# Kernel tuning notes

Measured on AMD Instinct MI355X. Metric: run time of the kernel, lower is better.

The kernel has to match this reference:

```python
import jax, jax.numpy as jnp
import numpy as np
import math

B, S, D = 2, 2048, 1024
H, KV, HD = 16, 4, 64
N_REP = H // KV
ROPE_THETA = 1.0e6


def _rope_tables(seq_len, head_dim, theta):
    inv_freq = 1.0 / (theta ** (np.arange(0, head_dim, 2, dtype=np.float32) / head_dim))
    t = np.arange(seq_len, dtype=np.float32)
    freqs = np.outer(t, inv_freq)                      # [S, HD/2]
    emb = np.concatenate([freqs, freqs], axis=-1)      # [S, HD]
    return jnp.asarray(np.cos(emb)), jnp.asarray(np.sin(emb))


def setup_inputs() -> dict:
    key = jax.random.key(0)
    ks = jax.random.split(key, 6)
    cos, sin = _rope_tables(S, HD, ROPE_THETA)
    scale = 0.02
    return {
        "x": jax.random.normal(ks[0], (B, S, D), dtype=jnp.float32),
        "cos": cos,
        "sin": sin,
        "Wq": jax.random.normal(ks[1], (D, H * HD), dtype=jnp.float32) * scale,
        "Wk": jax.random.normal(ks[2], (D, KV * HD), dtype=jnp.float32) * scale,
        "Wv": jax.random.normal(ks[3], (D, KV * HD), dtype=jnp.float32) * scale,
        "Wo": jax.random.normal(ks[4], (H * HD, D), dtype=jnp.float32) * scale,
    }


def _rotate_half(u):
    u1, u2 = u[..., : HD // 2], u[..., HD // 2 :]
    return jnp.concatenate([-u2, u1], axis=-1)


def reference(x, cos, sin, Wq, Wk, Wv, Wo):
    bsz, seq_len, _ = x.shape
    q = (x @ Wq).reshape(bsz, seq_len, H, HD)   # [B,S,H,HD]
    k = (x @ Wk).reshape(bsz, seq_len, KV, HD)  # [B,S,KV,HD]
    v = (x @ Wv).reshape(bsz, seq_len, KV, HD)

    # RoPE: cos/sin [S,HD] broadcast over batch and heads (unsqueeze_dim=1)
    c = cos[:seq_len][None, :, None, :]
    s = sin[:seq_len][None, :, None, :]
    q = q * c + _rotate_half(q) * s
    k = k * c + _rotate_half(k) * s

    # repeat_kv: expand KV heads groupwise to H heads
    k = jnp.repeat(k, N_REP, axis=2)  # [B,S,H,HD]
    v = jnp.repeat(v, N_REP, axis=2)

    q = q.transpose(0, 2, 1, 3)  # [B,H,S,HD]
    k = k.transpose(0, 2, 1, 3)
    v = v.transpose(0, 2, 1, 3)

    scores = jnp.einsum("bhqd,bhkd->bhqk", q, k) / math.sqrt(HD)
    causal = jnp.tril(jnp.ones((seq_len, seq_len), dtype=bool))
    scores = jnp.where(causal[None, None], scores, jnp.finfo(jnp.float32).min)
    probs = jax.nn.softmax(scores.astype(jnp.float32), axis=-1).astype(x.dtype)

    out = jnp.einsum("bhqk,bhkd->bhqd", probs, v)        # [B,H,S,HD]
    out = out.transpose(0, 2, 1, 3).reshape(bsz, seq_len, H * HD)
    return out @ Wo
```

## Files before the change

### kernel.cpp

```cpp
#include <hip/hip_runtime.h>

#define SS 2048
#define NH 16
#define NKV 4
#define HD 64

typedef __bf16 bf16;
typedef __bf16 bf16x8 __attribute__((ext_vector_type(8)));
typedef float f32x4 __attribute__((ext_vector_type(4)));

#define SM_SCALE 0.18033688011f

__device__ __forceinline__ void gl_lds16(const bf16* g, bf16* l) {
    __builtin_amdgcn_global_load_lds((const __attribute__((address_space(1))) void*)g,
                                     (__attribute__((address_space(3))) void*)l, 16, 0, 0);
}

__global__ __launch_bounds__(256) void prep_kernel(
    const float* __restrict__ x, const float* __restrict__ Wq, const float* __restrict__ Wk,
    const float* __restrict__ Wv, const float* __restrict__ Wo,
    bf16* __restrict__ xb, bf16* __restrict__ wqkv_t, bf16* __restrict__ wo_t)
{
    const int blk = blockIdx.x;
    const int tid = threadIdx.x;
    if (blk >= 640) {
        const float4* xv = (const float4*)x;
        const size_t base = (size_t)(blk - 640) * 2048 + tid;
        #pragma unroll
        for (int j = 0; j < 8; ++j) {
            const float4 v = xv[base + j * 256];
            bf16* o = xb + (base + j * 256) * 4;
            o[0] = (bf16)v.x; o[1] = (bf16)v.y; o[2] = (bf16)v.z; o[3] = (bf16)v.w;
        }
        return;
    }
    const float* W; bf16* Wt; int N, n0, k0;
    if (blk < 256)      { W = Wq; Wt = wqkv_t;                       N = 1024; n0 = (blk & 15) * 64;         k0 = (blk >> 4) * 64; }
    else if (blk < 320) { W = Wk; Wt = wqkv_t + (size_t)1024 * 1024; N = 256;  n0 = ((blk - 256) & 3) * 64;  k0 = ((blk - 256) >> 2) * 64; }
    else if (blk < 384) { W = Wv; Wt = wqkv_t + (size_t)1280 * 1024; N = 256;  n0 = ((blk - 320) & 3) * 64;  k0 = ((blk - 320) >> 2) * 64; }
    else                { W = Wo; Wt = wo_t;                         N = 1024; n0 = ((blk - 384) & 15) * 64; k0 = ((blk - 384) >> 4) * 64; }

    __shared__ float Ts[64][65];
    const int c = tid & 63, rr = tid >> 6;
    #pragma unroll
    for (int i = 0; i < 16; ++i) {
        const int kk = i * 4 + rr;
        Ts[kk][c] = W[(size_t)(k0 + kk) * N + n0 + c];
    }
    __syncthreads();
    #pragma unroll
    for (int i = 0; i < 16; ++i) {
        const int nn = i * 4 + rr;
        Wt[(size_t)(n0 + nn) * 1024 + k0 + c] = (bf16)Ts[c][nn];
    }
}

template<int EPI>
__global__ __launch_bounds__(512) void gemm_bt_kernel(
    const bf16* __restrict__ A, const bf16* __restrict__ Bt, float* __restrict__ C,
    const float* __restrict__ cosp, const float* __restrict__ sinp,
    bf16* __restrict__ qo, bf16* __restrict__ ko, bf16* __restrict__ vto,
    int M, int N, int K)
{
    __shared__ bf16 As[128 * 32];
    __shared__ bf16 Bs[128 * 32];
    const int m0 = blockIdx.x * 128, n0 = blockIdx.y * 128;
    const int tid = threadIdx.x;
    const int w = tid >> 6, lane = tid & 63, g = lane >> 4, li = lane & 15;
    const int wm = w >> 1, wn = w & 1;

    f32x4 acc[2][4];
    const f32x4 z = {0.f, 0.f, 0.f, 0.f};
    #pragma unroll
    for (int i = 0; i < 2; ++i)
        #pragma unroll
        for (int j = 0; j < 4; ++j) acc[i][j] = z;

    const int srow = tid >> 2, schunk = (tid & 3) * 8;
    const bf16* pA = A + (size_t)(m0 + srow) * K + schunk;
    const bf16* pB = Bt + (size_t)(n0 + srow) * K + schunk;
    bf16* lA = As + (size_t)w * 512;
    bf16* lB = Bs + (size_t)w * 512;

    for (int kk = 0; kk < K; kk += 32) {
        __syncthreads();
        gl_lds16(pA + kk, lA);
        gl_lds16(pB + kk, lB);
        __syncthreads();
        bf16x8 af[2], bfr[4];
        #pragma unroll
        for (int mi = 0; mi < 2; ++mi) af[mi] = *(const bf16x8*)&As[(wm * 32 + mi * 16 + li) * 32 + g * 8];
        #pragma unroll
        for (int ni = 0; ni < 4; ++ni) bfr[ni] = *(const bf16x8*)&Bs[(wn * 64 + ni * 16 + li) * 32 + g * 8];
        #pragma unroll
        for (int mi = 0; mi < 2; ++mi)
            #pragma unroll
            for (int ni = 0; ni < 4; ++ni)
                acc[mi][ni] = __builtin_amdgcn_mfma_f32_16x16x32_bf16(af[mi], bfr[ni], acc[mi][ni], 0, 0, 0);
    }

    const int row0 = m0 + wm * 32, col0 = n0 + wn * 64;
    if (EPI == 0) {
        #pragma unroll
        for (int mi = 0; mi < 2; ++mi)
            #pragma unroll
            for (int ni = 0; ni < 4; ++ni)
                #pragma unroll
                for (int r = 0; r < 4; ++r)
                    C[(size_t)(row0 + mi * 16 + g * 4 + r) * N + col0 + ni * 16 + li] = acc[mi][ni][r];
    } else {
        #pragma unroll
        for (int ni = 0; ni < 4; ++ni) {
            const int col = col0 + ni * 16 + li;
            const int d = col & 63;
            #pragma unroll
            for (int mi = 0; mi < 2; ++mi) {
                #pragma unroll
                for (int r = 0; r < 4; ++r) {
                    const int row = row0 + mi * 16 + g * 4 + r;
                    const int bb = row >> 11, s = row & 2047;
                    float val = acc[mi][ni][r];
                    if (col < 1280) {
                        const float pairv = acc[mi][ni ^ 2][r];
                        const float rot = (d < 32) ? -pairv : pairv;
                        val = val * cosp[s * 64 + d] + rot * sinp[s * 64 + d];
                    }
                    if (col < 1024) {
                        const int hh = col >> 6;
                        qo[(((size_t)bb * NH + hh) * SS + s) * HD + d] = (bf16)val;
                    } else if (col < 1280) {
                        const int kh = (col - 1024) >> 6;
                        ko[(((size_t)bb * NKV + kh) * SS + s) * HD + d] = (bf16)val;
                    } else {
                        const int kh = (col - 1280) >> 6;
                        vto[(((size_t)bb * NKV + kh) * HD + d) * SS + s] = (bf16)val;
                    }
                }
            }
        }
    }
}

#define FP 72
#define FPV 136
__global__ __launch_bounds__(256) void flash_kernel(const bf16* __restrict__ q, const bf16* __restrict__ k,
                                                    const bf16* __restrict__ vt, bf16* __restrict__ o)
{
    __shared__ bf16 Ks[128][FP];
    __shared__ bf16 Vt[64][FPV];
    __shared__ bf16 Ps[4][16][FP];

    const int blk = blockIdx.x;
    const int p = blk & 15;
    const int h = (blk >> 4) & 15;
    const int b = blk >> 8;
    const int kvh = h >> 2;
    const int tid = threadIdx.x;
    const int w = tid >> 6, lane = tid & 63, g = lane >> 4, li = lane & 15;

    const bf16* qh = q + ((size_t)b * NH + h) * SS * HD;
    const bf16* kh = k + ((size_t)b * NKV + kvh) * SS * HD;
    const bf16* vh = vt + ((size_t)b * NKV + kvh) * (size_t)HD * SS;

    bf16x8 ones;
    #pragma unroll
    for (int j = 0; j < 8; ++j) ones[j] = (bf16)1.0f;
    const f32x4 z = {0.f, 0.f, 0.f, 0.f};

    #pragma unroll
    for (int phase = 0; phase < 2; ++phase) {
        const int qt = phase ? p : (31 - p);

        const bf16* qrow = qh + (size_t)(qt * 64 + w * 16 + li) * HD;
        bf16x8 qf[2];
        qf[0] = *(const bf16x8*)(qrow + g * 8);
        qf[1] = *(const bf16x8*)(qrow + 32 + g * 8);

        f32x4 o_acc[4], l_acc;
        #pragma unroll
        for (int nt = 0; nt < 4; ++nt) o_acc[nt] = z;
        l_acc = z;

        for (int kt0 = 0; kt0 <= qt; kt0 += 2) {
            __syncthreads();
            {
                const int krow = tid >> 1, kcol = (tid & 1) * 32;
                const uint4* ks = (const uint4*)(kh + (size_t)(kt0 * 64 + krow) * HD + kcol);
                const uint4 a0 = ks[0], a1 = ks[1], a2 = ks[2], a3 = ks[3];
                *(uint4*)&Ks[krow][kcol]      = a0;
                *(uint4*)&Ks[krow][kcol + 8]  = a1;
                *(uint4*)&Ks[krow][kcol + 16] = a2;
                *(uint4*)&Ks[krow][kcol + 24] = a3;
                const int vrow = tid >> 2, vcol = (tid & 3) * 32;
                const uint4* vs = (const uint4*)(vh + (size_t)vrow * SS + kt0 * 64 + vcol);
                const uint4 c0 = vs[0], c1 = vs[1], c2 = vs[2], c3 = vs[3];
                *(uint4*)&Vt[vrow][vcol]      = c0;
                *(uint4*)&Vt[vrow][vcol + 8]  = c1;
                *(uint4*)&Vt[vrow][vcol + 16] = c2;
                *(uint4*)&Vt[vrow][vcol + 24] = c3;
            }
            __syncthreads();

            #pragma unroll
            for (int sub = 0; sub < 2; ++sub) {
                const int kt = kt0 + sub;
                if (kt > qt) break;

                f32x4 s_acc[4];
                #pragma unroll
                for (int nt = 0; nt < 4; ++nt) s_acc[nt] = z;
                #pragma unroll
                for (int t = 0; t < 2; ++t)
                    #pragma unroll
                    for (int nt = 0; nt < 4; ++nt) {
                        const bf16x8 kf = *(const bf16x8*)&Ks[sub * 64 + nt * 16 + li][t * 32 + g * 8];
                        s_acc[nt] = __builtin_amdgcn_mfma_f32_16x16x32_bf16(qf[t], kf, s_acc[nt], 0, 0, 0);
                    }

                const bool diag = (kt == qt);
                const int qr0 = qt * 64 + w * 16 + g * 4;
                #pragma unroll
                for (int nt = 0; nt < 4; ++nt) {
                    const int key = kt * 64 + nt * 16 + li;
                    #pragma unroll
                    for (int r = 0; r < 4; ++r) {
                        float sv = s_acc[nt][r] * SM_SCALE;
                        if (diag && key > qr0 + r) sv = -1e30f;
                        Ps[w][g * 4 + r][nt * 16 + li] = (bf16)exp2f(sv);
                    }
                }

                #pragma unroll
                for (int t = 0; t < 2; ++t) {
                    const bf16x8 pf = *(const bf16x8*)&Ps[w][li][t * 32 + g * 8];
                    l_acc = __builtin_amdgcn_mfma_f32_16x16x32_bf16(pf, ones, l_acc, 0, 0, 0);
                    #pragma unroll
                    for (int nt = 0; nt < 4; ++nt) {
                        const bf16x8 vf = *(const bf16x8*)&Vt[nt * 16 + li][sub * 64 + t * 32 + g * 8];
                        o_acc[nt] = __builtin_amdgcn_mfma_f32_16x16x32_bf16(pf, vf, o_acc[nt], 0, 0, 0);
                    }
                }
            }
        }

        #pragma unroll
        for (int r = 0; r < 4; ++r) {
            const float inv = 1.f / l_acc[r];
            const int s = qt * 64 + w * 16 + g * 4 + r;
            bf16* orow = o + (((size_t)b * SS + s) * NH + h) * HD;
            #pragma unroll
            for (int nt = 0; nt < 4; ++nt) orow[nt * 16 + li] = (bf16)(o_acc[nt][r] * inv);
        }
    }
}

extern "C" void kernel_launch(void* const* d_in, const int* in_sizes, int n_in,
                              void* d_out, int out_size, void* d_ws, size_t ws_size,
                              hipStream_t stream) {
    const float* x     = (const float*)d_in[0];
    const float* cos_t = (const float*)d_in[1];
    const float* sin_t = (const float*)d_in[2];
    const float* Wq    = (const float*)d_in[3];
    const float* Wk    = (const float*)d_in[4];
    const float* Wv    = (const float*)d_in[5];
    const float* Wo    = (const float*)d_in[6];
    float* out = (float*)d_out;

    char* wsb = (char*)d_ws;
    bf16* x_b    = (bf16*)(wsb);
    bf16* wqkv_t = (bf16*)(wsb + 8388608);
    bf16* wo_t   = (bf16*)(wsb + 11534336);
    bf16* q_b    = (bf16*)(wsb + 13631488);
    bf16* k_b    = (bf16*)(wsb + 22020096);
    bf16* vt_b   = (bf16*)(wsb + 24117248);
    bf16* o_b    = x_b;

    prep_kernel<<<1152, 256, 0, stream>>>(x, Wq, Wk, Wv, Wo, x_b, wqkv_t, wo_t);

    gemm_bt_kernel<2><<<dim3(32, 12), 512, 0, stream>>>(x_b, wqkv_t, nullptr, cos_t, sin_t,
                                                        q_b, k_b, vt_b, 4096, 1536, 1024);
    flash_kernel<<<512, 256, 0, stream>>>(q_b, k_b, vt_b, o_b);
    gemm_bt_kernel<0><<<dim3(32, 8), 512, 0, stream>>>(o_b, wo_t, out, nullptr, nullptr,
                                                       nullptr, nullptr, nullptr, 4096, 1024, 1024);
}
```

Measured before the change: 192.7 us.

## Double GEMM K-tile with XOR-swizzled LDS, fold softmax scale into Q

The GEMM K step grows from 32 to 64, with an XOR swizzle on the LDS tile layout to avoid bank conflicts, so each barrier pair now covers twice as many MFMAs. The softmax scale is folded into Q during the projection epilogue, which removes a per-score multiply in the flash kernel. Causal masking is split so only the diagonal tile pays for the comparisons. The P tile in LDS is also XOR-swizzled to cut bank conflicts. The risks are more LDS per GEMM block and an extra bf16 rounding of the scaled Q.

```diff
diff --git a/kernel.cpp b/kernel.cpp
--- a/kernel.cpp
+++ b/kernel.cpp
@@ -62,8 +62,8 @@
     bf16* __restrict__ qo, bf16* __restrict__ ko, bf16* __restrict__ vto,
     int M, int N, int K)
 {
-    __shared__ bf16 As[128 * 32];
-    __shared__ bf16 Bs[128 * 32];
+    __shared__ bf16 As[128 * 64];
+    __shared__ bf16 Bs[128 * 64];
     const int m0 = blockIdx.x * 128, n0 = blockIdx.y * 128;
     const int tid = threadIdx.x;
     const int w = tid >> 6, lane = tid & 63, g = lane >> 4, li = lane & 15;
@@ -76,27 +76,43 @@
         #pragma unroll
         for (int j = 0; j < 4; ++j) acc[i][j] = z;
 
-    const int srow = tid >> 2, schunk = (tid & 3) * 8;
-    const bf16* pA = A + (size_t)(m0 + srow) * K + schunk;
-    const bf16* pB = Bt + (size_t)(n0 + srow) * K + schunk;
-    bf16* lA = As + (size_t)w * 512;
-    bf16* lB = Bs + (size_t)w * 512;
-
-    for (int kk = 0; kk < K; kk += 32) {
+    const int srow = tid >> 3;
+    const int schunk = ((tid & 7) ^ (srow & 7)) * 8;
+    const bf16* pA0 = A + (size_t)(m0 + srow) * K + schunk;
+    const bf16* pA1 = A + (size_t)(m0 + 64 + srow) * K + schunk;
+    const bf16* pB0 = Bt + (size_t)(n0 + srow) * K + schunk;
+    const bf16* pB1 = Bt + (size_t)(n0 + 64 + srow) * K + schunk;
+    bf16* lA0 = As + (size_t)w * 512;
+    bf16* lA1 = As + 4096 + (size_t)w * 512;
+    bf16* lB0 = Bs + (size_t)w * 512;
+    bf16* lB1 = Bs + 4096 + (size_t)w * 512;
+
+    for (int kk = 0; kk < K; kk += 64) {
         __syncthreads();
-        gl_lds16(pA + kk, lA);
-        gl_lds16(pB + kk, lB);
+        gl_lds16(pA0 + kk, lA0);
+        gl_lds16(pA1 + kk, lA1);
+        gl_lds16(pB0 + kk, lB0);
+        gl_lds16(pB1 + kk, lB1);
         __syncthreads();
-        bf16x8 af[2], bfr[4];
-        #pragma unroll
-        for (int mi = 0; mi < 2; ++mi) af[mi] = *(const bf16x8*)&As[(wm * 32 + mi * 16 + li) * 32 + g * 8];
-        #pragma unroll
-        for (int ni = 0; ni < 4; ++ni) bfr[ni] = *(const bf16x8*)&Bs[(wn * 64 + ni * 16 + li) * 32 + g * 8];
-        #pragma unroll
-        for (int mi = 0; mi < 2; ++mi)
-            #pragma unroll
-            for (int ni = 0; ni < 4; ++ni)
-                acc[mi][ni] = __builtin_amdgcn_mfma_f32_16x16x32_bf16(af[mi], bfr[ni], acc[mi][ni], 0, 0, 0);
+        #pragma unroll
+        for (int t = 0; t < 2; ++t) {
+            bf16x8 af[2], bfr[4];
+            #pragma unroll
+            for (int mi = 0; mi < 2; ++mi) {
+                const int row = wm * 32 + mi * 16 + li;
+                af[mi] = *(const bf16x8*)&As[row * 64 + (((t * 4 + g) ^ (li & 7)) * 8)];
+            }
+            #pragma unroll
+            for (int ni = 0; ni < 4; ++ni) {
+                const int row = wn * 64 + ni * 16 + li;
+                bfr[ni] = *(const bf16x8*)&Bs[row * 64 + (((t * 4 + g) ^ (li & 7)) * 8)];
+            }
+            #pragma unroll
+            for (int mi = 0; mi < 2; ++mi)
+                #pragma unroll
+                for (int ni = 0; ni < 4; ++ni)
+                    acc[mi][ni] = __builtin_amdgcn_mfma_f32_16x16x32_bf16(af[mi], bfr[ni], acc[mi][ni], 0, 0, 0);
+        }
     }
 
     const int row0 = m0 + wm * 32, col0 = n0 + wn * 64;
@@ -127,7 +143,7 @@
                     }
                     if (col < 1024) {
                         const int hh = col >> 6;
-                        qo[(((size_t)bb * NH + hh) * SS + s) * HD + d] = (bf16)val;
+                        qo[(((size_t)bb * NH + hh) * SS + s) * HD + d] = (bf16)(val * SM_SCALE);
                     } else if (col < 1280) {
                         const int kh = (col - 1024) >> 6;
                         ko[(((size_t)bb * NKV + kh) * SS + s) * HD + d] = (bf16)val;
@@ -217,22 +233,29 @@
                         s_acc[nt] = __builtin_amdgcn_mfma_f32_16x16x32_bf16(qf[t], kf, s_acc[nt], 0, 0, 0);
                     }
 
-                const bool diag = (kt == qt);
-                const int qr0 = qt * 64 + w * 16 + g * 4;
-                #pragma unroll
-                for (int nt = 0; nt < 4; ++nt) {
-                    const int key = kt * 64 + nt * 16 + li;
+                if (kt == qt) {
+                    const int qr0 = qt * 64 + w * 16 + g * 4;
                     #pragma unroll
-                    for (int r = 0; r < 4; ++r) {
-                        float sv = s_acc[nt][r] * SM_SCALE;
-                        if (diag && key > qr0 + r) sv = -1e30f;
-                        Ps[w][g * 4 + r][nt * 16 + li] = (bf16)exp2f(sv);
-                    }
+                    for (int nt = 0; nt < 4; ++nt) {
+                        const int key = kt * 64 + nt * 16 + li;
+                        #pragma unroll
+                        for (int r = 0; r < 4; ++r) {
+                            float sv = s_acc[nt][r];
+                            if (key > qr0 + r) sv = -1e30f;
+                            Ps[w][g * 4 + r][(nt * 16 + li) ^ (g * 16)] = (bf16)exp2f(sv);
+                        }
+                    }
+                } else {
+                    #pragma unroll
+                    for (int nt = 0; nt < 4; ++nt)
+                        #pragma unroll
+                        for (int r = 0; r < 4; ++r)
+                            Ps[w][g * 4 + r][(nt * 16 + li) ^ (g * 16)] = (bf16)exp2f(s_acc[nt][r]);
                 }
 
                 #pragma unroll
                 for (int t = 0; t < 2; ++t) {
-                    const bf16x8 pf = *(const bf16x8*)&Ps[w][li][t * 32 + g * 8];
+                    const bf16x8 pf = *(const bf16x8*)&Ps[w][li][(t * 32 + g * 8) ^ ((li >> 2) * 16)];
                     l_acc = __builtin_amdgcn_mfma_f32_16x16x32_bf16(pf, ones, l_acc, 0, 0, 0);
                     #pragma unroll
                     for (int nt = 0; nt < 4; ++nt) {
```

Measured after the change: 179.6 us. -6.8%, faster.
